# Kernel optimization log

Hardware: AMD Instinct MI355X
Metric: run time of the kernel (lower is better)

Reference implementation:

```python
import jax, jax.numpy as jnp
import numpy as np

NUM_EMBEDDINGS = 1024
EMBEDDING_DIM = 256
COMMITMENT_COST = 0.02


def setup_inputs() -> dict:
    key = jax.random.key(0)
    k1, k2 = jax.random.split(key)
    z = jax.random.normal(k1, (64, 256, 32, 32), dtype=jnp.float32)
    # torch init: uniform(-1/K, 1/K)
    emb = jax.random.uniform(k2, (NUM_EMBEDDINGS, EMBEDDING_DIM), dtype=jnp.float32,
                             minval=-1.0 / NUM_EMBEDDINGS, maxval=1.0 / NUM_EMBEDDINGS)
    return {"z": z, "emb": emb}


def reference(z, emb):
    n, d, h, w = z.shape
    # (N, D, H, W) -> (N*H*W, D)
    z_flat = jnp.transpose(z, (0, 2, 3, 1)).reshape(-1, d)
    # squared L2 distances: ||z||^2 - 2 z.E^T + ||E||^2  -> (NHW, K)
    distances = (jnp.sum(z_flat * z_flat, axis=1, keepdims=True)
                 - 2.0 * z_flat @ emb.T
                 + jnp.sum(emb * emb, axis=1))
    indices = jnp.argmin(distances, axis=1)  # (NHW,)
    z_q = jnp.transpose(emb[indices].reshape(n, h, w, d), (0, 3, 1, 2))  # (N, D, H, W)
    # straight-through estimator
    z_q_st = z + jax.lax.stop_gradient(z_q - z)
    commitment_loss = COMMITMENT_COST * jnp.mean((jax.lax.stop_gradient(z) - z_q) ** 2)
    codebook_loss = jnp.mean((z - jax.lax.stop_gradient(z_q)) ** 2)
    vq_loss = commitment_loss + codebook_loss
    indices_reshaped = indices.reshape(n, h, w)
    return z_q_st, indices_reshaped, vq_loss
```

## Files before the change

kernel.cpp:

```cpp
#include <hip/hip_runtime.h>
#include <hip/hip_bf16.h>
#include <float.h>

#define OUT_IDX_OFF 16777216
#define OUT_LOSS_OFF 16842752
#define CAND_OFF 8388608
#define GMIN_OFF 12582912
#define GCNT_OFF 13107200
#define NSLOT 32
#define DELTA 2.0e-3f

typedef __attribute__((ext_vector_type(8))) short short8;
typedef __attribute__((ext_vector_type(4))) float f32x4;

static __device__ __forceinline__ unsigned short f2bf(float f) {
  union { __hip_bfloat16 h; unsigned short u; } cv;
  cv.h = __float2bfloat16(f);
  return cv.u;
}

__global__ __launch_bounds__(256) void k_prep(const float* __restrict__ emb,
                                              unsigned short* __restrict__ E2,
                                              float* __restrict__ cws) {
  const int k = blockIdx.x, d = threadIdx.x;
  const float v = emb[k * 256 + d];
  __shared__ float red[256];
  __shared__ unsigned short row[256];
  row[d] = f2bf(v);
  red[d] = v * v;
  __syncthreads();
  for (int s = 128; s > 0; s >>= 1) {
    if (d < s) red[d] += red[d + s];
    __syncthreads();
  }
  if (d == 0) cws[k] = red[0];
  if (d < 32) ((short8*)&E2[k * 256])[d] = ((short8*)row)[d];
}

__global__ __launch_bounds__(256) void k_cvt4(const float* __restrict__ z,
                                              unsigned short* __restrict__ A2,
                                              float* __restrict__ aws) {
#pragma clang fp contract(off)
  __shared__ float tile[64][65];
  __shared__ float red2[128];
  const int t = threadIdx.x;
  const int p0 = blockIdx.x << 6;
  const int n = p0 >> 10, hw0 = p0 & 1023;
  const float* zb = z + (size_t)n * 262144 + hw0;
  const int hwl = (t & 15) << 2;
  const int dlb = t >> 4;
  const int row = t & 63, h = (t >> 6) & 1;
  const int pl = t >> 2, c = t & 3;

  float4 v[4];
#pragma unroll
  for (int i = 0; i < 4; ++i)
    v[i] = *(const float4*)&zb[(size_t)(dlb + i * 16) * 1024 + hwl];

  float acc[8];

  for (int dt = 0; dt < 4; ++dt) {
    if (dt) __syncthreads();
#pragma unroll
    for (int i = 0; i < 4; ++i) {
      const int dl = dlb + i * 16;
      tile[hwl + 0][dl] = v[i].x;
      tile[hwl + 1][dl] = v[i].y;
      tile[hwl + 2][dl] = v[i].z;
      tile[hwl + 3][dl] = v[i].w;
    }
    __syncthreads();
    if (dt < 3) {
      const float* zb2 = zb + (size_t)(dt + 1) * 65536;
#pragma unroll
      for (int i = 0; i < 4; ++i)
        v[i] = *(const float4*)&zb2[(size_t)(dlb + i * 16) * 1024 + hwl];
    }
    unsigned short* dst = &A2[(size_t)(p0 + pl) * 256 + dt * 64];
#pragma unroll
    for (int hh = 0; hh < 2; ++hh) {
      const int ch = c + hh * 4;
      unsigned short tmp[8];
#pragma unroll
      for (int j = 0; j < 8; ++j) tmp[j] = f2bf(tile[pl][ch * 8 + j]);
      *(short8*)&dst[ch * 8] = *(short8*)tmp;
    }
    if (t < 128 && (dt >> 1) == h) {
      if ((dt & 1) == 0) {
#pragma unroll
        for (int j = 0; j < 8; ++j) {
          const float x = tile[row][j];
          acc[j] = x * x;
        }
        for (int g = 1; g < 8; ++g)
#pragma unroll
          for (int j = 0; j < 8; ++j) {
            const float x = tile[row][g * 8 + j];
            const float p = x * x;
            acc[j] = acc[j] + p;
          }
      } else {
        for (int g = 8; g < 16; ++g)
#pragma unroll
          for (int j = 0; j < 8; ++j) {
            const float x = tile[row][(g - 8) * 8 + j];
            const float p = x * x;
            acc[j] = acc[j] + p;
          }
      }
    }
  }
  if (t < 128) {
    const float s = ((acc[0] + acc[1]) + (acc[2] + acc[3])) +
                    ((acc[4] + acc[5]) + (acc[6] + acc[7]));
    red2[t] = s;
  }
  __syncthreads();
  if (t < 64) aws[p0 + t] = red2[t] + red2[t + 64];
}

__global__ __launch_bounds__(256, 2) void k_gemm6(
    const unsigned short* __restrict__ A2, const unsigned short* __restrict__ E2,
    const float* __restrict__ cws, const float* __restrict__ aws,
    int* __restrict__ gmin, int* __restrict__ gcnt,
    float2* __restrict__ gcand) {
  __shared__ __align__(16) unsigned short As[2][8192];
  __shared__ __align__(16) unsigned short Bs[2][8192];
  __shared__ float a_l[128], c_l[128], rmkt[256], bmin[128];

  const int t = threadIdx.x;
  const int lane = t & 63;
  const int wave = __builtin_amdgcn_readfirstlane(t >> 6);
  const int wr = wave >> 1, wc = wave & 1;
  const int quad = lane >> 4, l15 = lane & 15;
  const int swa = l15 & 7;

  const int bid = blockIdx.x;
  const int L = ((bid & 7) << 9) + (bid >> 3);
  const int rb = L >> 3, ck = L & 7;
  const int r0 = rb << 7, k0 = ck << 7;

  if (t < 128) {
    a_l[t] = aws[r0 + t];
    c_l[t] = cws[k0 + t];
  }

  const int srow = t >> 3;
  const int gpos = t & 7;

  f32x4 acc[4][4];
#pragma unroll
  for (int a = 0; a < 4; ++a)
#pragma unroll
    for (int b = 0; b < 4; ++b) acc[a][b] = (f32x4)(0.0f);

  auto stage = [&](int kt, int buf) {
#pragma unroll
    for (int i = 0; i < 4; ++i) {
      const int row = (i << 5) + srow;
      const int gsrc = gpos ^ (row & 7);
      const unsigned short* sa =
          A2 + (((size_t)(r0 + row)) << 8) + (kt << 6) + (gsrc << 3);
      __builtin_amdgcn_global_load_lds(
          (const __attribute__((address_space(1))) void*)sa,
          (__attribute__((address_space(3))) void*)(&As[buf][0] + (i << 11) +
                                                    (wave << 9)),
          16, 0, 0);
      const unsigned short* sb =
          E2 + (((size_t)(k0 + row)) << 8) + (kt << 6) + (gsrc << 3);
      __builtin_amdgcn_global_load_lds(
          (const __attribute__((address_space(1))) void*)sb,
          (__attribute__((address_space(3))) void*)(&Bs[buf][0] + (i << 11) +
                                                    (wave << 9)),
          16, 0, 0);
    }
  };

  stage(0, 0);
  __syncthreads();

#pragma unroll
  for (int kt = 0; kt < 4; ++kt) {
    if (kt < 3) stage(kt + 1, (kt + 1) & 1);
    const unsigned short* as = &As[kt & 1][0];
    const unsigned short* bs = &Bs[kt & 1][0];
#pragma unroll
    for (int ks = 0; ks < 2; ++ks) {
      short8 af[4], bf[4];
#pragma unroll
      for (int tr = 0; tr < 4; ++tr)
        af[tr] = *(const short8*)&as[(wr * 64 + tr * 16 + l15) * 64 +
                                     (((ks * 4 + quad) ^ swa) << 3)];
#pragma unroll
      for (int tc = 0; tc < 4; ++tc)
        bf[tc] = *(const short8*)&bs[(wc * 64 + tc * 16 + l15) * 64 +
                                     (((ks * 4 + quad) ^ swa) << 3)];
#pragma unroll
      for (int tr = 0; tr < 4; ++tr)
#pragma unroll
        for (int tc = 0; tc < 4; ++tc)
          acc[tr][tc] = __builtin_amdgcn_mfma_f32_16x16x32_bf16(
              af[tr], bf[tc], acc[tr][tc], 0, 0, 0);
    }
    __syncthreads();
  }

#pragma unroll
  for (int tr = 0; tr < 4; ++tr)
#pragma unroll
    for (int rg = 0; rg < 4; ++rg) {
      const int rloc = wr * 64 + tr * 16 + quad * 4 + rg;
      const float av = a_l[rloc];
      float mn = FLT_MAX;
#pragma unroll
      for (int tc = 0; tc < 4; ++tc) {
        const int cloc = wc * 64 + tc * 16 + l15;
        const float s = av + fmaf(-2.0f, acc[tr][tc][rg], c_l[cloc]);
        mn = fminf(mn, s);
      }
      mn = fminf(mn, __shfl_xor(mn, 1));
      mn = fminf(mn, __shfl_xor(mn, 2));
      mn = fminf(mn, __shfl_xor(mn, 4));
      mn = fminf(mn, __shfl_xor(mn, 8));
      if (l15 == 0) rmkt[rloc * 2 + wc] = mn;
    }
  __syncthreads();
  if (t < 128) {
    const float m = fminf(rmkt[t * 2], rmkt[t * 2 + 1]);
    const int old = atomicMin(&gmin[r0 + t], __float_as_int(m));
    bmin[t] = fminf(m, __int_as_float(old));
  }
  __syncthreads();
#pragma unroll
  for (int tr = 0; tr < 4; ++tr)
#pragma unroll
    for (int rg = 0; rg < 4; ++rg) {
      const int rloc = wr * 64 + tr * 16 + quad * 4 + rg;
      const float av = a_l[rloc];
      const float lim = bmin[rloc] + DELTA;
#pragma unroll
      for (int tc = 0; tc < 4; ++tc) {
        const int cloc = wc * 64 + tc * 16 + l15;
        const float s = av + fmaf(-2.0f, acc[tr][tc][rg], c_l[cloc]);
        if (s <= lim) {
          const int pos = atomicAdd(&gcnt[r0 + rloc], 1);
          if (pos < NSLOT)
            gcand[(size_t)(r0 + rloc) * NSLOT + pos] =
                make_float2(s, __int_as_float(k0 + cloc));
        }
      }
    }
}

__global__ __launch_bounds__(256) void k_finish(
    const float* __restrict__ z, const float* __restrict__ emb,
    const float* __restrict__ cws, const float* __restrict__ aws,
    const int* __restrict__ gmin, const int* __restrict__ gcnt,
    const float2* __restrict__ gcand, int* __restrict__ idxws,
    float* __restrict__ out) {
  const int tid = (blockIdx.x << 8) + threadIdx.x;
  const int r = tid >> 2, sub = tid & 3;
  const float lim = __int_as_float(gmin[r]) + DELTA;
  int m = gcnt[r];
  if (m > NSLOT) m = NSLOT;
  const int n = r >> 10, hw = r & 1023;
  const float* zp = z + (size_t)n * 262144 + hw;
  const float a = aws[r];
  float bestv = FLT_MAX;
  int besti = 0x7fffffff;
  for (int ci = sub; ci < m; ci += 4) {
    const float2 p = gcand[(size_t)r * NSLOT + ci];
    if (p.x > lim) continue;
    const int k = __float_as_int(p.y);
    const float* ep = emb + (size_t)k * 256;
    float dot = 0.0f;
#pragma unroll 8
    for (int d = 0; d < 256; ++d) dot = fmaf(zp[(size_t)d * 1024], ep[d], dot);
    float s = fmaf(-2.0f, dot, a);
    s = s + cws[k];
    if (s < bestv || (s == bestv && k < besti)) {
      bestv = s;
      besti = k;
    }
  }
#pragma unroll
  for (int off = 1; off < 4; off <<= 1) {
    const float ov = __shfl_xor(bestv, off);
    const int oi = __shfl_xor(besti, off);
    if (ov < bestv || (ov == bestv && oi < besti)) {
      bestv = ov;
      besti = oi;
    }
  }
  if (sub == 0) {
    idxws[r] = besti;
    out[OUT_IDX_OFF + r] = (float)besti;
  }
  float c = (sub == 0) ? bestv : 0.0f;
#pragma unroll
  for (int off = 1; off < 64; off <<= 1) c += __shfl_xor(c, off);
  if ((threadIdx.x & 63) == 0)
    atomicAdd(&out[OUT_LOSS_OFF], c * (1.02f / 16777216.0f));
}

__global__ __launch_bounds__(256) void k_out2(const float* __restrict__ emb,
                                              const int* __restrict__ idxws,
                                              float* __restrict__ out) {
  __shared__ float zq[32][257];
  __shared__ int sidx[32];
  const int t = threadIdx.x;
  const int p0 = blockIdx.x << 5;
  const int n = p0 >> 10, hw0 = p0 & 1023;
  if (t < 32) sidx[t] = idxws[p0 + t];
  __syncthreads();
#pragma unroll
  for (int it = 0; it < 8; ++it) {
    const int i = t + (it << 8);
    const int p = i >> 6;
    const int q = (i & 63) << 2;
    const float4 v = *(const float4*)&emb[(size_t)sidx[p] * 256 + q];
    zq[p][q] = v.x;
    zq[p][q + 1] = v.y;
    zq[p][q + 2] = v.z;
    zq[p][q + 3] = v.w;
  }
  __syncthreads();
  const int p = t & 31, d0 = t >> 5;
  float* ob = out + (size_t)n * 262144 + hw0 + p;
#pragma unroll
  for (int dd = 0; dd < 32; ++dd) {
    const int d = (dd << 3) + d0;
    ob[(size_t)d * 1024] = zq[p][d];
  }
}

extern "C" void kernel_launch(void* const* d_in, const int* in_sizes, int n_in,
                              void* d_out, int out_size, void* d_ws,
                              size_t ws_size, hipStream_t stream) {
  const float* z = (const float*)d_in[0];
  const float* emb = (const float*)d_in[1];
  float* out = (float*)d_out;

  unsigned short* E2 = (unsigned short*)d_ws;
  float* cws = (float*)(E2 + 262144);
  float* aws = cws + 1024;
  int* idxws = (int*)(aws + 65536);
  unsigned short* A2 = (unsigned short*)d_out;
  float2* gcand = (float2*)(out + CAND_OFF);
  int* gmin = (int*)(out + GMIN_OFF);
  int* gcnt = (int*)(out + GCNT_OFF);

  hipMemsetAsync((char*)d_out + (size_t)OUT_LOSS_OFF * 4, 0, 4, stream);
  hipMemsetAsync(gmin, 0x7f, 65536 * 4, stream);
  hipMemsetAsync(gcnt, 0, 65536 * 4, stream);

  k_prep<<<dim3(1024), dim3(256), 0, stream>>>(emb, E2, cws);
  k_cvt4<<<dim3(1024), dim3(256), 0, stream>>>(z, A2, aws);
  k_gemm6<<<dim3(4096), dim3(256), 0, stream>>>(A2, E2, cws, aws, gmin, gcnt,
                                                gcand);
  k_finish<<<dim3(1024), dim3(256), 0, stream>>>(z, emb, cws, aws, gmin, gcnt,
                                                 gcand, idxws, out);
  k_out2<<<dim3(2048), dim3(256), 0, stream>>>(emb, idxws, out);
}
```

Before: 354.1 us.

## Single-buffer GEMM LDS and alias epilogue scratch to raise occupancy

The distance GEMM kernel drops double-buffered LDS staging for a single 32KB buffer and reuses it for the epilogue reduction scratch. The per-block row and codebook norms are now read straight from global memory instead of being staged in LDS. Launch bounds go from 2 to 5 blocks per CU, so more waves can hide latency. In exchange, loads no longer overlap with MFMA inside a block, which adds a barrier per k-step, and register pressure under the tighter bound may cause spills.

```diff
diff --git a/kernel.cpp b/kernel.cpp
--- a/kernel.cpp
+++ b/kernel.cpp
@@ -119,14 +119,16 @@
   if (t < 64) aws[p0 + t] = red2[t] + red2[t + 64];
 }
 
-__global__ __launch_bounds__(256, 2) void k_gemm6(
+__global__ __launch_bounds__(256, 5) void k_gemm7(
     const unsigned short* __restrict__ A2, const unsigned short* __restrict__ E2,
     const float* __restrict__ cws, const float* __restrict__ aws,
     int* __restrict__ gmin, int* __restrict__ gcnt,
     float2* __restrict__ gcand) {
-  __shared__ __align__(16) unsigned short As[2][8192];
-  __shared__ __align__(16) unsigned short Bs[2][8192];
-  __shared__ float a_l[128], c_l[128], rmkt[256], bmin[128];
+  __shared__ __align__(16) unsigned short smem[16384];
+  unsigned short* As = smem;
+  unsigned short* Bs = smem + 8192;
+  float* rmkt = (float*)smem;
+  float* bmin = ((float*)smem) + 256;
 
   const int t = threadIdx.x;
   const int lane = t & 63;
@@ -140,11 +142,6 @@
   const int rb = L >> 3, ck = L & 7;
   const int r0 = rb << 7, k0 = ck << 7;
 
-  if (t < 128) {
-    a_l[t] = aws[r0 + t];
-    c_l[t] = cws[k0 + t];
-  }
-
   const int srow = t >> 3;
   const int gpos = t & 7;
 
@@ -154,7 +151,8 @@
 #pragma unroll
     for (int b = 0; b < 4; ++b) acc[a][b] = (f32x4)(0.0f);
 
-  auto stage = [&](int kt, int buf) {
+  for (int kt = 0; kt < 4; ++kt) {
+    if (kt) __syncthreads();
 #pragma unroll
     for (int i = 0; i < 4; ++i) {
       const int row = (i << 5) + srow;
@@ -163,37 +161,28 @@
           A2 + (((size_t)(r0 + row)) << 8) + (kt << 6) + (gsrc << 3);
       __builtin_amdgcn_global_load_lds(
           (const __attribute__((address_space(1))) void*)sa,
-          (__attribute__((address_space(3))) void*)(&As[buf][0] + (i << 11) +
+          (__attribute__((address_space(3))) void*)(As + (i << 11) +
                                                     (wave << 9)),
           16, 0, 0);
       const unsigned short* sb =
           E2 + (((size_t)(k0 + row)) << 8) + (kt << 6) + (gsrc << 3);
       __builtin_amdgcn_global_load_lds(
           (const __attribute__((address_space(1))) void*)sb,
-          (__attribute__((address_space(3))) void*)(&Bs[buf][0] + (i << 11) +
+          (__attribute__((address_space(3))) void*)(Bs + (i << 11) +
                                                     (wave << 9)),
           16, 0, 0);
     }
-  };
-
-  stage(0, 0);
-  __syncthreads();
-
-#pragma unroll
-  for (int kt = 0; kt < 4; ++kt) {
-    if (kt < 3) stage(kt + 1, (kt + 1) & 1);
-    const unsigned short* as = &As[kt & 1][0];
-    const unsigned short* bs = &Bs[kt & 1][0];
+    __syncthreads();
 #pragma unroll
     for (int ks = 0; ks < 2; ++ks) {
       short8 af[4], bf[4];
 #pragma unroll
       for (int tr = 0; tr < 4; ++tr)
-        af[tr] = *(const short8*)&as[(wr * 64 + tr * 16 + l15) * 64 +
+        af[tr] = *(const short8*)&As[(wr * 64 + tr * 16 + l15) * 64 +
                                      (((ks * 4 + quad) ^ swa) << 3)];
 #pragma unroll
       for (int tc = 0; tc < 4; ++tc)
-        bf[tc] = *(const short8*)&bs[(wc * 64 + tc * 16 + l15) * 64 +
+        bf[tc] = *(const short8*)&Bs[(wc * 64 + tc * 16 + l15) * 64 +
                                      (((ks * 4 + quad) ^ swa) << 3)];
 #pragma unroll
       for (int tr = 0; tr < 4; ++tr)
@@ -202,20 +191,20 @@
           acc[tr][tc] = __builtin_amdgcn_mfma_f32_16x16x32_bf16(
               af[tr], bf[tc], acc[tr][tc], 0, 0, 0);
     }
-    __syncthreads();
-  }
+  }
+  __syncthreads();
 
 #pragma unroll
   for (int tr = 0; tr < 4; ++tr)
 #pragma unroll
     for (int rg = 0; rg < 4; ++rg) {
       const int rloc = wr * 64 + tr * 16 + quad * 4 + rg;
-      const float av = a_l[rloc];
+      const float av = aws[r0 + rloc];
       float mn = FLT_MAX;
 #pragma unroll
       for (int tc = 0; tc < 4; ++tc) {
         const int cloc = wc * 64 + tc * 16 + l15;
-        const float s = av + fmaf(-2.0f, acc[tr][tc][rg], c_l[cloc]);
+        const float s = av + fmaf(-2.0f, acc[tr][tc][rg], cws[k0 + cloc]);
         mn = fminf(mn, s);
       }
       mn = fminf(mn, __shfl_xor(mn, 1));
@@ -236,12 +225,12 @@
 #pragma unroll
     for (int rg = 0; rg < 4; ++rg) {
       const int rloc = wr * 64 + tr * 16 + quad * 4 + rg;
-      const float av = a_l[rloc];
+      const float av = aws[r0 + rloc];
       const float lim = bmin[rloc] + DELTA;
 #pragma unroll
       for (int tc = 0; tc < 4; ++tc) {
         const int cloc = wc * 64 + tc * 16 + l15;
-        const float s = av + fmaf(-2.0f, acc[tr][tc][rg], c_l[cloc]);
+        const float s = av + fmaf(-2.0f, acc[tr][tc][rg], cws[k0 + cloc]);
         if (s <= lim) {
           const int pos = atomicAdd(&gcnt[r0 + rloc], 1);
           if (pos < NSLOT)
@@ -356,7 +345,7 @@
 
   k_prep<<<dim3(1024), dim3(256), 0, stream>>>(emb, E2, cws);
   k_cvt4<<<dim3(1024), dim3(256), 0, stream>>>(z, A2, aws);
-  k_gemm6<<<dim3(4096), dim3(256), 0, stream>>>(A2, E2, cws, aws, gmin, gcnt,
+  k_gemm7<<<dim3(4096), dim3(256), 0, stream>>>(A2, E2, cws, aws, gmin, gcnt,
                                                 gcand);
   k_finish<<<dim3(1024), dim3(256), 0, stream>>>(z, emb, cws, aws, gmin, gcnt,
                                                  gcand, idxws, out);
```

New measurement: 458.9 us. 29.6% more time.
